# Performance work log

Hardware: AMD Instinct MI355X
Metric: run time of the kernel (lower is better)

The kernel has to match this reference:

```python
import jax, jax.numpy as jnp
import numpy as np

N_QUBITS = 12
DEPTH = 2
TOPOLOGY = 'ring'
N_FEATURES = 12
BATCH = 4096
DIM = 2 ** N_QUBITS


def _apply_ry(state, theta):
    # state: [B, left, 2, right] caller-reshaped; here take [B, 2**n] + qubit index
    return state


def apply_ry(state, theta, q):
    # RY(theta) = [[cos(t/2), -sin(t/2)], [sin(t/2), cos(t/2)]], shared across batch
    c, s = jnp.cos(theta / 2), jnp.sin(theta / 2)
    G = jnp.stack([jnp.stack([c, -s]), jnp.stack([s, c])])  # [2, 2]
    left = 2 ** q
    right = 2 ** (N_QUBITS - q - 1)
    st = state.reshape(-1, left, 2, right)
    st = jnp.einsum('ab,xlbr->xlar', G, st)
    return st.reshape(state.shape)


def apply_cnot(state, c, t):
    # flip target axis on the control=1 half of the statevector
    B = state.shape[0]
    st = state.reshape((B,) + (2,) * N_QUBITS)
    c_ax, t_ax = 1 + c, 1 + t
    s0 = jnp.take(st, 0, axis=c_ax)
    s1 = jnp.take(st, 1, axis=c_ax)
    t_adj = t_ax if t < c else t_ax - 1  # axis shift after removing control axis
    s1 = jnp.flip(s1, axis=t_adj)
    st = jnp.stack([s0, s1], axis=c_ax)
    return st.reshape(B, DIM)


def circuit_features(x, weights):
    B = x.shape[0]
    # initial layer: RY(x[i % n_features]) on |0> per qubit -> product state
    idx = np.arange(N_QUBITS) % N_FEATURES
    half = x[:, idx] / 2  # [B, n_qubits]
    state = jnp.ones((B, 1), dtype=x.dtype)
    for i in range(N_QUBITS):
        v = jnp.stack([jnp.cos(half[:, i]), jnp.sin(half[:, i])], axis=1)  # [B, 2]
        state = (state[:, :, None] * v[:, None, :]).reshape(B, -1)
    # entangling + trainable RY layers
    for l in range(DEPTH):
        if TOPOLOGY == 'ring':
            pairs = [(i, (i + 1) % N_QUBITS) for i in range(N_QUBITS)]
        elif TOPOLOGY == 'chain':
            pairs = [(i, i + 1) for i in range(N_QUBITS - 1)]
        else:  # all2all
            pairs = [(i, j) for i in range(N_QUBITS) for j in range(i + 1, N_QUBITS)]
        for (ci, ti) in pairs:
            state = apply_cnot(state, ci, ti)
        for i in range(N_QUBITS):
            state = apply_ry(state, weights[l, i], i)
    # <Z_i> = sum_b |amp_b|^2 * (1 - 2*bit_i(b)); qubit 0 is most significant
    probs = state * state  # [B, 2^n], state is real
    bits = (np.arange(DIM)[None, :] >> (N_QUBITS - 1 - np.arange(N_QUBITS))[:, None]) & 1
    signs = jnp.asarray(1.0 - 2.0 * bits, dtype=x.dtype)  # [n_qubits, 2^n]
    return probs @ signs.T  # [B, n_qubits]


def setup_inputs() -> dict:
    key = jax.random.key(0)
    kx, kw, kW, kb = jax.random.split(key, 4)
    x = jax.random.normal(kx, (BATCH, N_FEATURES), dtype=jnp.float32)
    weights = jax.random.normal(kw, (DEPTH, N_QUBITS), dtype=jnp.float32)
    W = jax.random.normal(kW, (2, N_QUBITS), dtype=jnp.float32) / np.sqrt(N_QUBITS)
    b = jnp.zeros((2,), dtype=jnp.float32)
    return {"x": x, "weights": weights, "W": W, "b": b}


def reference(x, weights, W, b):
    feats = circuit_features(x, weights)  # [B, n_qubits]
    return feats @ W.T + b  # [B, 2]
```

## Files before the change

kernel.cpp:

```cpp
#include <hip/hip_runtime.h>
#include <hip/hip_bf16.h>

#define NQ 12
typedef __hip_bfloat16 bf16;
typedef float v2f __attribute__((ext_vector_type(2)));

__device__ __forceinline__ float b2f(unsigned int u) {
  union { unsigned int i; float f; } v; v.i = u << 16; return v.f;
}

__device__ __forceinline__ float ldv(const void* p, int i, bool f32) {
  if (f32) return ((const float*)p)[i];
  return b2f((unsigned int)((const unsigned short*)p)[i]);
}

__device__ __forceinline__ int ringperm(int d) {
  int a = d ^ ((d & 1) << 11);
  return a ^ (a >> 1);
}

__device__ __forceinline__ int swz(int p) { return p ^ ((p >> 6) & 31); }

__global__ __launch_bounds__(64) void qsim_kernel(
    const void* __restrict__ x,
    const void* __restrict__ w,
    const void* __restrict__ Wm,
    const void* __restrict__ bv,
    void* __restrict__ out)
{
  __shared__ float st[4096];
  const int lane = threadIdx.x;
  const int b = blockIdx.x;

  bool f32;
  {
    const unsigned short* xu = (const unsigned short*)x;
    int insane = 0;
#pragma unroll
    for (int i = 0; i < 16; ++i) {
      float v = b2f((unsigned int)xu[2 * i]);
      float a = fabsf(v);
      if (!(a <= 64.f) || (a != 0.f && a < 1e-8f)) ++insane;
    }
    f32 = (insane >= 2);
  }

  v2f amp[32];
  {
    float csx[12], snx[12];
#pragma unroll
    for (int q = 0; q < 12; ++q) {
      float h = 0.5f * ldv(x, b * NQ + q, f32);
      csx[q] = __cosf(h); snx[q] = __sinf(h);
    }
    const int rb = ringperm(lane << 6);
    float f0[12], f1[12];
#pragma unroll
    for (int q = 0; q < 12; ++q) {
      int r = (rb >> (11 - q)) & 1;
      f0[q] = r ? snx[q] : csx[q];
      f1[q] = r ? csx[q] : snx[q];
    }
    const float K   = f0[2] * f0[3] * f0[4] * f0[5];
    const float h0f = f0[0] * f0[1];
    const float h1f = f1[0] * f1[1];
    const float u00 = f0[11] * h0f, u01 = f1[11] * h1f;
    const float u10 = f1[11] * h0f, u11 = f0[11] * h1f;
#pragma unroll
    for (int j5 = 0; j5 < 2; ++j5) {
      const float a5 = K * (j5 ? f1[6] : f0[6]);
#pragma unroll
      for (int j4 = 0; j4 < 2; ++j4) {
        const float a4 = a5 * ((j4 ^ j5) ? f1[7] : f0[7]);
#pragma unroll
        for (int j3 = 0; j3 < 2; ++j3) {
          const float a3 = a4 * ((j3 ^ j4) ? f1[8] : f0[8]);
#pragma unroll
          for (int j2 = 0; j2 < 2; ++j2) {
            const float a2 = a3 * ((j2 ^ j3) ? f1[9] : f0[9]);
#pragma unroll
            for (int j1 = 0; j1 < 2; ++j1) {
              const float a1 = a2 * ((j1 ^ j2) ? f1[10] : f0[10]);
              const int k = (j5 << 4) | (j4 << 3) | (j3 << 2) | (j2 << 1) | j1;
              amp[k].x = a1 * (j1 ? u10 : u00);
              amp[k].y = a1 * (j1 ? u11 : u01);
            }
          }
        }
      }
    }
  }

  const int rb1 = swz(ringperm(lane << 6));
  const int wb2 = (lane << 6) ^ (lane & 31);

#pragma unroll 1
  for (int l = 0; l < 2; ++l) {
    if (l) {
      __syncthreads();
#pragma unroll
      for (int j = 0; j < 64; ++j)
        st[((j << 6) ^ (j & 31)) ^ lane] = amp[j >> 1][j & 1];
      __syncthreads();
#pragma unroll
      for (int j = 0; j < 64; ++j)
        amp[j >> 1][j & 1] = st[rb1 ^ swz(ringperm(j))];
    }

#pragma unroll
    for (int q = 6; q < 11; ++q) {
      float h = 0.5f * ldv(w, l * NQ + q, f32);
      const float c = __cosf(h), s = __sinf(h);
      const int hm = 1 << (10 - q);
#pragma unroll
      for (int k = 0; k < 32; ++k) {
        if (k & hm) continue;
        v2f v0 = amp[k], v1 = amp[k | hm];
        amp[k]      = c * v0 - s * v1;
        amp[k | hm] = s * v0 + c * v1;
      }
    }
    {
      float h = 0.5f * ldv(w, l * NQ + 11, f32);
      const float c = __cosf(h), s = __sinf(h);
#pragma unroll
      for (int k = 0; k < 32; ++k) {
        float xx = amp[k].x, yy = amp[k].y;
        amp[k].x = fmaf(c, xx, -s * yy);
        amp[k].y = fmaf(s, xx,  c * yy);
      }
    }

    __syncthreads();
#pragma unroll
    for (int j = 0; j < 64; ++j)
      st[wb2 ^ j] = amp[j >> 1][j & 1];
    __syncthreads();
#pragma unroll
    for (int j = 0; j < 64; ++j)
      amp[j >> 1][j & 1] = st[((j << 6) ^ (j & 31)) ^ lane];

#pragma unroll
    for (int q = 0; q < 5; ++q) {
      float h = 0.5f * ldv(w, l * NQ + q, f32);
      const float c = __cosf(h), s = __sinf(h);
      const int hm = 1 << (4 - q);
#pragma unroll
      for (int k = 0; k < 32; ++k) {
        if (k & hm) continue;
        v2f v0 = amp[k], v1 = amp[k | hm];
        amp[k]      = c * v0 - s * v1;
        amp[k | hm] = s * v0 + c * v1;
      }
    }
    {
      float h = 0.5f * ldv(w, l * NQ + 5, f32);
      const float c = __cosf(h), s = __sinf(h);
#pragma unroll
      for (int k = 0; k < 32; ++k) {
        float xx = amp[k].x, yy = amp[k].y;
        amp[k].x = fmaf(c, xx, -s * yy);
        amp[k].y = fmaf(s, xx,  c * yy);
      }
    }
  }

  v2f Pv = {0.f, 0.f}, zv0 = Pv, zv1 = Pv, zv2 = Pv, zv3 = Pv, zv4 = Pv;
  float z5 = 0.f;
#pragma unroll
  for (int k = 0; k < 32; ++k) {
    v2f pr = amp[k] * amp[k];
    Pv += pr;
    zv0 += (k & 16) ? -pr : pr;
    zv1 += (k & 8)  ? -pr : pr;
    zv2 += (k & 4)  ? -pr : pr;
    zv3 += (k & 2)  ? -pr : pr;
    zv4 += (k & 1)  ? -pr : pr;
    z5  += pr.x - pr.y;
  }
  const float P  = Pv.x + Pv.y;
  const float z0 = zv0.x + zv0.y, z1 = zv1.x + zv1.y, z2 = zv2.x + zv2.y;
  const float z3 = zv3.x + zv3.y, z4 = zv4.x + zv4.y;

  float t0, t1;
#pragma unroll
  for (int r = 0; r < 2; ++r) {
    float acc = z0 * ldv(Wm, r * NQ + 0, f32) + z1 * ldv(Wm, r * NQ + 1, f32)
              + z2 * ldv(Wm, r * NQ + 2, f32) + z3 * ldv(Wm, r * NQ + 3, f32)
              + z4 * ldv(Wm, r * NQ + 4, f32) + z5 * ldv(Wm, r * NQ + 5, f32);
    float wsum = 0.f;
#pragma unroll
    for (int q = 6; q < 12; ++q) {
      float wv = ldv(Wm, r * NQ + q, f32);
      wsum += ((lane >> (11 - q)) & 1) ? -wv : wv;
    }
    acc = fmaf(P, wsum, acc);
    if (r == 0) t0 = acc; else t1 = acc;
  }
#pragma unroll
  for (int off = 32; off; off >>= 1) {
    t0 += __shfl_xor(t0, off, 64);
    t1 += __shfl_xor(t1, off, 64);
  }
  if (lane < 2) {
    float o = ((lane == 0) ? t0 : t1) + ldv(bv, lane, f32);
    if (f32) ((float*)out)[b * 2 + lane] = o;
    else     ((bf16*)out)[b * 2 + lane] = __float2bfloat16(o);
  }
}

extern "C" void kernel_launch(void* const* d_in, const int* in_sizes, int n_in,
                              void* d_out, int out_size, void* d_ws, size_t ws_size,
                              hipStream_t stream) {
  const void* x  = d_in[0];
  const void* w  = d_in[1];
  const void* Wm = d_in[2];
  const void* bv = d_in[3];
  const int batch = out_size / 2;
  qsim_kernel<<<dim3(batch), dim3(64), 0, stream>>>(x, w, Wm, bv, d_out);
}
```

Baseline: 87.44 us.

## Fold final RY layer into observable and use shear-form rotations

The second layer's RY gates are no longer applied to the state. Each <Z_q> after RY is rewritten as cos(theta)<Z> - sin(theta)<X>, and the <X> expectations are computed from pairwise amplitude products after the entangling permutation. The remaining RY gates are applied as three-shear (tan/sin) updates, which need fewer multiplies each. This replaces the second layer's rotation arithmetic with correlation sums plus an extra shared-memory transpose, and the shear form may change rounding slightly.

After: 85.94 us. No clear change (-1.7%).

```diff
diff --git a/kernel.cpp b/kernel.cpp
--- a/kernel.cpp
+++ b/kernel.cpp
@@ -94,75 +94,113 @@
   const int rb1 = swz(ringperm(lane << 6));
   const int wb2 = (lane << 6) ^ (lane & 31);
 
-#pragma unroll 1
-  for (int l = 0; l < 2; ++l) {
-    if (l) {
-      __syncthreads();
-#pragma unroll
-      for (int j = 0; j < 64; ++j)
-        st[((j << 6) ^ (j & 31)) ^ lane] = amp[j >> 1][j & 1];
-      __syncthreads();
-#pragma unroll
-      for (int j = 0; j < 64; ++j)
-        amp[j >> 1][j & 1] = st[rb1 ^ swz(ringperm(j))];
-    }
-
-#pragma unroll
-    for (int q = 6; q < 11; ++q) {
-      float h = 0.5f * ldv(w, l * NQ + q, f32);
-      const float c = __cosf(h), s = __sinf(h);
-      const int hm = 1 << (10 - q);
-#pragma unroll
-      for (int k = 0; k < 32; ++k) {
-        if (k & hm) continue;
-        v2f v0 = amp[k], v1 = amp[k | hm];
-        amp[k]      = c * v0 - s * v1;
-        amp[k | hm] = s * v0 + c * v1;
-      }
-    }
-    {
-      float h = 0.5f * ldv(w, l * NQ + 11, f32);
-      const float c = __cosf(h), s = __sinf(h);
-#pragma unroll
-      for (int k = 0; k < 32; ++k) {
-        float xx = amp[k].x, yy = amp[k].y;
-        amp[k].x = fmaf(c, xx, -s * yy);
-        amp[k].y = fmaf(s, xx,  c * yy);
-      }
-    }
-
-    __syncthreads();
-#pragma unroll
-    for (int j = 0; j < 64; ++j)
-      st[wb2 ^ j] = amp[j >> 1][j & 1];
-    __syncthreads();
-#pragma unroll
-    for (int j = 0; j < 64; ++j)
-      amp[j >> 1][j & 1] = st[((j << 6) ^ (j & 31)) ^ lane];
-
-#pragma unroll
-    for (int q = 0; q < 5; ++q) {
-      float h = 0.5f * ldv(w, l * NQ + q, f32);
-      const float c = __cosf(h), s = __sinf(h);
-      const int hm = 1 << (4 - q);
-#pragma unroll
-      for (int k = 0; k < 32; ++k) {
-        if (k & hm) continue;
-        v2f v0 = amp[k], v1 = amp[k | hm];
-        amp[k]      = c * v0 - s * v1;
-        amp[k | hm] = s * v0 + c * v1;
-      }
-    }
-    {
-      float h = 0.5f * ldv(w, l * NQ + 5, f32);
-      const float c = __cosf(h), s = __sinf(h);
-#pragma unroll
-      for (int k = 0; k < 32; ++k) {
-        float xx = amp[k].x, yy = amp[k].y;
-        amp[k].x = fmaf(c, xx, -s * yy);
-        amp[k].y = fmaf(s, xx,  c * yy);
-      }
-    }
+#pragma unroll
+  for (int q = 6; q < 11; ++q) {
+    float h = 0.5f * ldv(w, 0 * NQ + q, f32);
+    const float t = __tanf(0.5f * h), s = __sinf(h);
+    const int hm = 1 << (10 - q);
+#pragma unroll
+    for (int k = 0; k < 32; ++k) {
+      if (k & hm) continue;
+      amp[k]      += -t * amp[k | hm];
+      amp[k | hm] +=  s * amp[k];
+      amp[k]      += -t * amp[k | hm];
+    }
+  }
+  {
+    float h = 0.5f * ldv(w, 0 * NQ + 11, f32);
+    const float t = __tanf(0.5f * h), s = __sinf(h);
+#pragma unroll
+    for (int k = 0; k < 32; ++k) {
+      amp[k].x = fmaf(-t, amp[k].y, amp[k].x);
+      amp[k].y = fmaf( s, amp[k].x, amp[k].y);
+      amp[k].x = fmaf(-t, amp[k].y, amp[k].x);
+    }
+  }
+
+  __syncthreads();
+#pragma unroll
+  for (int j = 0; j < 64; ++j)
+    st[wb2 ^ j] = amp[j >> 1][j & 1];
+  __syncthreads();
+#pragma unroll
+  for (int j = 0; j < 64; ++j)
+    amp[j >> 1][j & 1] = st[((j << 6) ^ (j & 31)) ^ lane];
+
+#pragma unroll
+  for (int q = 0; q < 5; ++q) {
+    float h = 0.5f * ldv(w, 0 * NQ + q, f32);
+    const float t = __tanf(0.5f * h), s = __sinf(h);
+    const int hm = 1 << (4 - q);
+#pragma unroll
+    for (int k = 0; k < 32; ++k) {
+      if (k & hm) continue;
+      amp[k]      += -t * amp[k | hm];
+      amp[k | hm] +=  s * amp[k];
+      amp[k]      += -t * amp[k | hm];
+    }
+  }
+  {
+    float h = 0.5f * ldv(w, 0 * NQ + 5, f32);
+    const float t = __tanf(0.5f * h), s = __sinf(h);
+#pragma unroll
+    for (int k = 0; k < 32; ++k) {
+      amp[k].x = fmaf(-t, amp[k].y, amp[k].x);
+      amp[k].y = fmaf( s, amp[k].x, amp[k].y);
+      amp[k].x = fmaf(-t, amp[k].y, amp[k].x);
+    }
+  }
+
+  __syncthreads();
+#pragma unroll
+  for (int j = 0; j < 64; ++j)
+    st[((j << 6) ^ (j & 31)) ^ lane] = amp[j >> 1][j & 1];
+  __syncthreads();
+#pragma unroll
+  for (int j = 0; j < 64; ++j)
+    amp[j >> 1][j & 1] = st[rb1 ^ swz(ringperm(j))];
+
+  float xB6, xB7, xB8, xB9, xB10, xB11;
+  {
+    v2f a6 = {0.f, 0.f}, a7 = a6, a8 = a6, a9 = a6, a10 = a6;
+    float a11 = 0.f;
+#pragma unroll
+    for (int k = 0; k < 32; ++k) {
+      a6  += amp[k] * amp[k ^ 16];
+      a7  += amp[k] * amp[k ^ 8];
+      a8  += amp[k] * amp[k ^ 4];
+      a9  += amp[k] * amp[k ^ 2];
+      a10 += amp[k] * amp[k ^ 1];
+      a11 += amp[k].x * amp[k].y;
+    }
+    xB6 = a6.x + a6.y; xB7 = a7.x + a7.y; xB8 = a8.x + a8.y;
+    xB9 = a9.x + a9.y; xB10 = a10.x + a10.y; xB11 = 2.f * a11;
+  }
+
+  __syncthreads();
+#pragma unroll
+  for (int j = 0; j < 64; ++j)
+    st[wb2 ^ j] = amp[j >> 1][j & 1];
+  __syncthreads();
+#pragma unroll
+  for (int j = 0; j < 64; ++j)
+    amp[j >> 1][j & 1] = st[((j << 6) ^ (j & 31)) ^ lane];
+
+  float xA0, xA1, xA2, xA3, xA4, xA5;
+  {
+    v2f a0 = {0.f, 0.f}, a1 = a0, a2 = a0, a3 = a0, a4 = a0;
+    float a5 = 0.f;
+#pragma unroll
+    for (int k = 0; k < 32; ++k) {
+      a0 += amp[k] * amp[k ^ 16];
+      a1 += amp[k] * amp[k ^ 8];
+      a2 += amp[k] * amp[k ^ 4];
+      a3 += amp[k] * amp[k ^ 2];
+      a4 += amp[k] * amp[k ^ 1];
+      a5 += amp[k].x * amp[k].y;
+    }
+    xA0 = a0.x + a0.y; xA1 = a1.x + a1.y; xA2 = a2.x + a2.y;
+    xA3 = a3.x + a3.y; xA4 = a4.x + a4.y; xA5 = 2.f * a5;
   }
 
   v2f Pv = {0.f, 0.f}, zv0 = Pv, zv1 = Pv, zv2 = Pv, zv3 = Pv, zv4 = Pv;
@@ -182,17 +220,31 @@
   const float z0 = zv0.x + zv0.y, z1 = zv1.x + zv1.y, z2 = zv2.x + zv2.y;
   const float z3 = zv3.x + zv3.y, z4 = zv4.x + zv4.y;
 
+  float ct[12], sn[12];
+#pragma unroll
+  for (int q = 0; q < 12; ++q) {
+    float th = ldv(w, NQ + q, f32);
+    ct[q] = __cosf(th); sn[q] = __sinf(th);
+  }
+  const float zA[6] = {z0, z1, z2, z3, z4, z5};
+  const float xA[6] = {xA0, xA1, xA2, xA3, xA4, xA5};
+  const float xB[6] = {xB6, xB7, xB8, xB9, xB10, xB11};
+
   float t0, t1;
 #pragma unroll
   for (int r = 0; r < 2; ++r) {
-    float acc = z0 * ldv(Wm, r * NQ + 0, f32) + z1 * ldv(Wm, r * NQ + 1, f32)
-              + z2 * ldv(Wm, r * NQ + 2, f32) + z3 * ldv(Wm, r * NQ + 3, f32)
-              + z4 * ldv(Wm, r * NQ + 4, f32) + z5 * ldv(Wm, r * NQ + 5, f32);
-    float wsum = 0.f;
+    float acc = 0.f, wsum = 0.f;
+#pragma unroll
+    for (int q = 0; q < 6; ++q) {
+      float wv = ldv(Wm, r * NQ + q, f32);
+      acc = fmaf(wv, fmaf(ct[q], zA[q], -sn[q] * xA[q]), acc);
+    }
 #pragma unroll
     for (int q = 6; q < 12; ++q) {
       float wv = ldv(Wm, r * NQ + q, f32);
-      wsum += ((lane >> (11 - q)) & 1) ? -wv : wv;
+      float wc = wv * ct[q];
+      wsum += ((lane >> (11 - q)) & 1) ? -wc : wc;
+      acc = fmaf(-wv * sn[q], xB[q - 6], acc);
     }
     acc = fmaf(P, wsum, acc);
     if (r == 0) t0 = acc; else t1 = acc;
```
